# Performance work log

Hardware: AMD Instinct MI355X
Metric: run time of the kernel (lower is better)

## Reference

```python
import jax, jax.numpy as jnp
import numpy as np
import math

B, L, DIM = 2, 2048, 1024
HEADS = 16
DH = DIM // HEADS  # 64
M_IALSH = 2
U_IALSH = 0.75
NEG = -1e4  # additive mask value for non-matching hash buckets


def setup_inputs() -> dict:
    key = jax.random.key(0)
    k0, k1, k2, k3 = jax.random.split(key, 4)
    return {
        "hidden_states": jax.random.normal(k0, (B, L, DIM), jnp.float32),
        "qk_w": jax.random.normal(k1, (DIM, DIM), jnp.float32) * 0.02,
        "qk_b": jnp.zeros((DIM,), jnp.float32),
        "v_w": jax.random.normal(k2, (DIM, DIM), jnp.float32) * 0.02,
        "v_b": jnp.zeros((DIM,), jnp.float32),
        "hash_a": jax.random.normal(k3, (DH + M_IALSH,), jnp.float32),
    }


def _ialsh_mask(qkh, hash_a):
    # qkh: (b, h, l, dh). IALSH (Improved Asymmetric LSH for MIPS):
    # keys scaled so max norm per (b,h) is U; P(x)=[x, 1/2-||x||^2, 1/2-||x||^4]
    # queries unit-normalized;        Q(x)=[x/||x||, 0, 0]
    norms = jnp.linalg.norm(qkh, axis=-1, keepdims=True)          # (b,h,l,1)
    max_norm = jnp.max(norms, axis=2, keepdims=True)              # (b,h,1,1)
    xk = qkh * (U_IALSH / jnp.maximum(max_norm, 1e-12))
    nk2 = jnp.sum(xk * xk, axis=-1, keepdims=True)                # ||x||^2
    P = jnp.concatenate([xk, 0.5 - nk2, 0.5 - nk2 * nk2], axis=-1)
    q_unit = qkh / jnp.maximum(norms, 1e-12)
    zeros = jnp.zeros_like(nk2)
    Q = jnp.concatenate([q_unit, zeros, zeros], axis=-1)
    hq = (Q @ hash_a) >= 0.0                                      # (b,h,l) sign hash
    hk = (P @ hash_a) >= 0.0
    same = hq[..., :, None] == hk[..., None, :]                   # (b,h,l,l)
    return jnp.where(same, 0.0, NEG).astype(qkh.dtype)


def reference(hidden_states, qk_w, qk_b, v_w, v_b, hash_a):
    b, l, d = hidden_states.shape
    qk = hidden_states @ qk_w.T + qk_b                            # shared Q/K projection
    v = hidden_states @ v_w.T + v_b

    def split(x):  # (b,l,d) -> (b,h,l,dh)
        return x.reshape(b, l, HEADS, DH).transpose(0, 2, 1, 3)

    qkh, vh = split(qk), split(v)
    scores = jnp.einsum('bhqd,bhkd->bhqk', qkh, qkh) / math.sqrt(DH)
    scores = scores + _ialsh_mask(qkh, hash_a)
    probs = jax.nn.softmax(scores, axis=-1)  # dropout = identity (eval mode)
    ctx = jnp.einsum('bhqk,bhkd->bhqd', probs, vh)
    return ctx.transpose(0, 2, 1, 3).reshape(b, l, d)
```

## Files before the change

### kernel.cpp

```cpp
#include <hip/hip_runtime.h>

typedef unsigned short u16;
typedef unsigned char  u8;
typedef unsigned int   u32;
typedef unsigned long long u64;

typedef short bf16x8 __attribute__((ext_vector_type(8)));
typedef float f32x4  __attribute__((ext_vector_type(4)));
typedef float f32x16 __attribute__((ext_vector_type(16)));

#define DEV __device__ __forceinline__

#if __has_builtin(__builtin_amdgcn_exp2f)
#define EXP2(x) __builtin_amdgcn_exp2f(x)
#else
#define EXP2(x) exp2f(x)
#endif

DEV u16 f2bf(float x) {
  u32 u = __builtin_bit_cast(u32, x);
  u32 r = (u + 0x7fffu + ((u >> 16) & 1u)) >> 16;
  return (u16)r;
}
DEV float bf2f(u16 h) {
  u32 u = ((u32)h) << 16;
  return __builtin_bit_cast(float, u);
}
DEV f32x4 mfma16(bf16x8 a, bf16x8 b, f32x4 c) {
  return __builtin_amdgcn_mfma_f32_16x16x32_bf16(a, b, c, 0, 0, 0);
}
DEV f32x16 mfma32(bf16x8 a, bf16x8 b, f32x16 c) {
  return __builtin_amdgcn_mfma_f32_32x32x16_bf16(a, b, c, 0, 0, 0);
}
DEV u32 cvtpk(float lo, float hi) {
  u32 r;
  asm("v_cvt_pk_bf16_f32 %0, %1, %2" : "=v"(r) : "v"(lo), "v"(hi));
  return r;
}
DEV void pswap(u32& x, u32& y) {
  asm("v_permlane32_swap_b32 %0, %1" : "+v"(x), "+v"(y));
}
DEV bf16x8 mkfrag(u32 w0, u32 w1, u32 w2, u32 w3) {
  union { u32 w[4]; bf16x8 v; } u;
  u.w[0] = w0; u.w[1] = w1; u.w[2] = w2; u.w[3] = w3;
  return u.v;
}

#define GLDS(gptr, lptr)                                                  \
  __builtin_amdgcn_global_load_lds(                                       \
      (const __attribute__((address_space(1))) void*)(gptr),              \
      (__attribute__((address_space(3))) void*)(lptr), 16, 0, 0)

__global__ __launch_bounds__(256) void split3_kernel(
    const float* __restrict__ hid, const float* __restrict__ wq,
    const float* __restrict__ wv,
    u16* __restrict__ hHi, u16* __restrict__ hLo,
    u16* __restrict__ wqHi, u16* __restrict__ wqLo, u16* __restrict__ wvHi) {
  const int NH = 4194304, NW = 1048576;
  int i = blockIdx.x * 256 + threadIdx.x;
  if (i < NH) {
    float v = hid[i];
    u16 t = f2bf(v);
    hHi[i] = t;
    hLo[i] = f2bf(v - bf2f(t));
  } else if (i < NH + NW) {
    int j = i - NH;
    float v = wq[j];
    u16 t = f2bf(v);
    wqHi[j] = t;
    wqLo[j] = f2bf(v - bf2f(t));
  } else {
    int j = i - NH - NW;
    wvHi[j] = f2bf(wv[j]);
  }
}

__global__ __launch_bounds__(256) void ca_kernel(
    const float* __restrict__ W, const float* __restrict__ ha, double* __restrict__ ca) {
  int idx = blockIdx.x * 256 + threadIdx.x;
  int h = idx >> 10, k = idx & 1023;
  double s = 0.0;
#pragma unroll 8
  for (int j = 0; j < 64; ++j)
    s += (double)W[(size_t)(h * 64 + j) * 1024 + k] * (double)ha[j];
  ca[idx] = s;
}

__global__ __launch_bounds__(256) void d_kernel(
    const float* __restrict__ hid, const double* __restrict__ ca, float* __restrict__ dq) {
  const int row0 = blockIdx.x * 8 + (threadIdx.x >> 6) * 2;
  const int lane = threadIdx.x & 63;
  double a0[16], a1[16];
#pragma unroll
  for (int h = 0; h < 16; ++h) { a0[h] = 0.0; a1[h] = 0.0; }
  const float* hp = hid + (size_t)row0 * 1024;
  for (int k = lane; k < 1024; k += 64) {
    const double h0 = (double)hp[k];
    const double h1 = (double)hp[k + 1024];
#pragma unroll
    for (int h = 0; h < 16; ++h) {
      const double c = ca[h * 1024 + k];
      a0[h] += h0 * c;
      a1[h] += h1 * c;
    }
  }
#pragma unroll
  for (int h = 0; h < 16; ++h) {
    double v0 = a0[h], v1 = a1[h];
#pragma unroll
    for (int off = 32; off; off >>= 1) {
      v0 += __shfl_xor(v0, off, 64);
      v1 += __shfl_xor(v1, off, 64);
    }
    if (lane == 0) {
      const int b0 = row0 >> 11, l0 = row0 & 2047;
      dq[(size_t)(b0 * 16 + h) * 2048 + l0] = (float)v0;
      const int r1 = row0 + 1;
      dq[(size_t)((r1 >> 11) * 16 + h) * 2048 + (r1 & 2047)] = (float)v1;
    }
  }
}

__global__ __launch_bounds__(256, 2) void gemm_fused(
    const u16* __restrict__ hHi, const u16* __restrict__ hLo,
    const u16* __restrict__ wqHi, const u16* __restrict__ wqLo,
    const u16* __restrict__ wvHi,
    const float* __restrict__ qk_b, const float* __restrict__ v_b,
    u16* __restrict__ qkB, u16* __restrict__ vT, float* __restrict__ n2A) {
  constexpr int K = 1024;
  __shared__ u16 S[2][16384];
  const int tid = threadIdx.x, wave = tid >> 6, lane = tid & 63;
  const int quad = lane >> 4, lm = lane & 15;
  const int wr = wave >> 1, wc = wave & 1;
  const int m0 = blockIdx.x * 64, n0 = blockIdx.y * 128;
  const int ch = lane & 3, rA = lane >> 2;

  auto stage = [&](int kt, int buf) {
    const int k0 = kt * 32;
    const int rowA = wave * 16 + rA;
    GLDS(hHi + (size_t)(m0 + rowA) * K + k0 + ch * 8, &S[buf][0 + wave * 512]);
    GLDS(hLo + (size_t)(m0 + rowA) * K + k0 + ch * 8, &S[buf][2048 + wave * 512]);
#pragma unroll
    for (int it = 0; it < 2; ++it) {
      const int rb = wave * 2 + it;
      const int row = rb * 16 + rA;
      GLDS(wqHi + (size_t)(n0 + row) * K + k0 + ch * 8, &S[buf][4096 + rb * 512]);
      GLDS(wqLo + (size_t)(n0 + row) * K + k0 + ch * 8, &S[buf][8192 + rb * 512]);
      GLDS(wvHi + (size_t)(n0 + row) * K + k0 + ch * 8, &S[buf][12288 + rb * 512]);
    }
  };

  f32x4 aq[2][4], av[4][2];
#pragma unroll
  for (int i = 0; i < 2; ++i)
#pragma unroll
    for (int j = 0; j < 4; ++j) aq[i][j] = {0.f, 0.f, 0.f, 0.f};
#pragma unroll
  for (int i = 0; i < 4; ++i)
#pragma unroll
    for (int j = 0; j < 2; ++j) av[i][j] = {0.f, 0.f, 0.f, 0.f};

  stage(0, 0);
  __syncthreads();

  for (int kt = 0; kt < 32; ++kt) {
    const int cur = kt & 1;
    if (kt < 31) stage(kt + 1, cur ^ 1);

    bf16x8 a_h[2], a_l[2], b_h[4], b_l[4], w_h[4];
#pragma unroll
    for (int i = 0; i < 2; ++i) {
      a_h[i] = *(const bf16x8*)&S[cur][(wr * 32 + i * 16 + lm) * 32 + quad * 8];
      a_l[i] = *(const bf16x8*)&S[cur][2048 + (wr * 32 + i * 16 + lm) * 32 + quad * 8];
    }
#pragma unroll
    for (int j = 0; j < 4; ++j) {
      b_h[j] = *(const bf16x8*)&S[cur][4096 + (wc * 64 + j * 16 + lm) * 32 + quad * 8];
      b_l[j] = *(const bf16x8*)&S[cur][8192 + (wc * 64 + j * 16 + lm) * 32 + quad * 8];
      w_h[j] = *(const bf16x8*)&S[cur][12288 + (wc * 64 + j * 16 + lm) * 32 + quad * 8];
    }
#pragma unroll
    for (int i = 0; i < 2; ++i)
#pragma unroll
      for (int j = 0; j < 4; ++j) {
        aq[i][j] = mfma16(a_h[i], b_h[j], aq[i][j]);
        aq[i][j] = mfma16(a_h[i], b_l[j], aq[i][j]);
        aq[i][j] = mfma16(a_l[i], b_h[j], aq[i][j]);
      }
#pragma unroll
    for (int iv = 0; iv < 4; ++iv)
#pragma unroll
      for (int jv = 0; jv < 2; ++jv)
        av[iv][jv] = mfma16(w_h[iv], a_h[jv], av[iv][jv]);

    __syncthreads();
  }

  const int hidx = blockIdx.y * 2 + wc;
#pragma unroll
  for (int i = 0; i < 2; ++i) {
    float nn[4] = {0.f, 0.f, 0.f, 0.f};
#pragma unroll
    for (int j = 0; j < 4; ++j) {
      const int col = n0 + wc * 64 + j * 16 + lm;
      const float bv = qk_b[col];
#pragma unroll
      for (int r = 0; r < 4; ++r) {
        const int row = m0 + wr * 32 + i * 16 + quad * 4 + r;
        const float val = aq[i][j][r] + bv;
        qkB[(size_t)row * 1024 + col] = f2bf(val);
        nn[r] += val * val;
      }
    }
#pragma unroll
    for (int r = 0; r < 4; ++r)
#pragma unroll
      for (int off = 1; off < 16; off <<= 1) nn[r] += __shfl_xor(nn[r], off, 64);
    if (lm == 0) {
      const int row = m0 + wr * 32 + i * 16 + quad * 4;
      const int b = row >> 11, l = row & 2047;
      *(float4*)&n2A[(size_t)(b * 16 + hidx) * 2048 + l] =
          make_float4(nn[0], nn[1], nn[2], nn[3]);
    }
  }
#pragma unroll
  for (int iv = 0; iv < 4; ++iv)
#pragma unroll
    for (int r = 0; r < 4; ++r) {
      const int vcol = n0 + wc * 64 + iv * 16 + quad * 4 + r;
      const float bv = v_b[vcol];
#pragma unroll
      for (int jv = 0; jv < 2; ++jv) {
        const int tok = m0 + wr * 32 + jv * 16 + lm;
        vT[(size_t)vcol * 4096 + tok] = f2bf(av[iv][jv][r] + bv);
      }
    }
}

__global__ __launch_bounds__(256) void bits_kernel(
    const float* __restrict__ n2A, const float* __restrict__ dq,
    const float* __restrict__ ha, u8* __restrict__ hqA, u64* __restrict__ hkM) {
  const int bh = blockIdx.x;
  const int tid = threadIdx.x;
  const int wave = tid >> 6, lane = tid & 63;
  __shared__ float red[4];
  const float* n2p = n2A + (size_t)bh * 2048;
  float4 v0 = ((const float4*)n2p)[tid];
  float4 v1 = ((const float4*)n2p)[tid + 256];
  float lmax = fmaxf(fmaxf(fmaxf(v0.x, v0.y), fmaxf(v0.z, v0.w)),
                     fmaxf(fmaxf(v1.x, v1.y), fmaxf(v1.z, v1.w)));
#pragma unroll
  for (int off = 1; off < 64; off <<= 1) lmax = fmaxf(lmax, __shfl_xor(lmax, off, 64));
  if (lane == 0) red[wave] = lmax;
  __syncthreads();
  const float maxn2 = fmaxf(fmaxf(red[0], red[1]), fmaxf(red[2], red[3]));
  const float s = 0.75f / fmaxf(sqrtf(maxn2), 1e-12f);
  const float a64 = ha[64], a65 = ha[65];
#pragma unroll
  for (int it = 0; it < 8; ++it) {
    const int l = it * 256 + tid;
    const float dv = dq[(size_t)bh * 2048 + l];
    const float n2 = n2p[l];
    const float nk2 = s * s * n2;
    const float hkdot = s * dv + (0.5f - nk2) * a64 + (0.5f - nk2 * nk2) * a65;
    hqA[(size_t)bh * 2048 + l] = (dv >= 0.f) ? 1 : 0;
    const u64 m = __ballot(hkdot >= 0.f);
    if (lane == 0) hkM[(size_t)bh * 32 + it * 4 + wave] = m;
  }
}

__global__ __launch_bounds__(128, 2) void attn_kernel(
    const u16* __restrict__ qkb, const u16* __restrict__ vT,
    const u8* __restrict__ hqA, const u64* __restrict__ hkM,
    float* __restrict__ out) {
  __shared__ u16 Ks[2][4096];
  __shared__ u16 Vs[2][4096];

  const int id = blockIdx.x;
  const int bh = id & 31, qt = id >> 5;
  const int b = bh >> 4, h = bh & 15;
  const int tid = threadIdx.x, wave = tid >> 6, lane = tid & 63;
  const int col = lane & 31;
  const int hf = lane >> 5;
  const int ch7 = col & 7;
  const int r8 = lane >> 3, ch = lane & 7;
  const int q0 = qt * 64;
  const int token = q0 + wave * 32 + col;

  const u16* qbase = qkb + (size_t)b * 2048 * 1024 + h * 64;
  const u16* vtb = vT + (size_t)h * 64 * 4096 + b * 2048;
  const u64* hkp = hkM + (size_t)bh * 32;

  bf16x8 aQ[4];
#pragma unroll
  for (int c = 0; c < 4; ++c)
    aQ[c] = *(const bf16x8*)(qbase + (size_t)token * 1024 + c * 16 + hf * 8);
  const u32 hqx = hqA[(size_t)bh * 2048 + token] ? 0xFFFFFFFFu : 0u;

  const int srow = wave * 32;
  auto stage = [&](int kt, int buf) {
#pragma unroll
    for (int i = 0; i < 4; ++i) {
      const int row = srow + i * 8 + r8;
      const int sw = (ch ^ (row & 7)) * 8;
      GLDS(qbase + (size_t)(kt * 64 + row) * 1024 + sw, &Ks[buf][(srow + i * 8) * 64]);
      GLDS(vtb + (size_t)row * 4096 + kt * 64 + sw, &Vs[buf][(srow + i * 8) * 64]);
    }
  };

  f32x16 acc[2];
  f32x16 accLv;
#pragma unroll
  for (int r = 0; r < 16; ++r) { acc[0][r] = 0.f; acc[1][r] = 0.f; accLv[r] = 0.f; }
  const bf16x8 ones = {0x3F80, 0x3F80, 0x3F80, 0x3F80, 0x3F80, 0x3F80, 0x3F80, 0x3F80};

  const float SCL = 0.18033688f;
  const float M0 = -4.3280854f;

  u64 mk = hkp[0];
  stage(0, 0);
  __syncthreads();

  for (int kt = 0; kt < 32; ++kt) {
    const int cur = kt & 1;
    if (kt < 31) stage(kt + 1, cur ^ 1);
    const u64 mk_next = (kt < 31) ? hkp[kt + 1] : 0ull;

    const u64 msh = mk >> (hf * 4);
    u32 mw[2];
    mw[0] = (u32)msh;
    mw[1] = (u32)(msh >> 32);

#pragma unroll
    for (int kb = 0; kb < 2; ++kb) {
      const u32 hw = mw[kb] ^ hqx;
      f32x16 cs;
#pragma unroll
      for (int r = 0; r < 16; ++r) cs[r] = 0.f;
#pragma unroll
      for (int c = 0; c < 4; ++c) {
        const bf16x8 aK = *(const bf16x8*)
            &Ks[cur][(kb * 32 + col) * 64 + (((c * 2 + hf) ^ ch7) * 8)];
        cs = mfma32(aK, aQ[c], cs);
      }
      u32 pk[8];
#pragma unroll
      for (int i = 0; i < 8; ++i) {
        const int r0 = 2 * i, r1 = 2 * i + 1;
        const int pos0 = (r0 & 3) + 8 * (r0 >> 2);
        const int pos1 = (r1 & 3) + 8 * (r1 >> 2);
        float p0 = EXP2(__builtin_fmaf(cs[r0], SCL, M0));
        float p1 = EXP2(__builtin_fmaf(cs[r1], SCL, M0));
        p0 = ((hw >> pos0) & 1u) ? 0.f : p0;
        p1 = ((hw >> pos1) & 1u) ? 0.f : p1;
        pk[i] = cvtpk(p0, p1);
      }
      pswap(pk[0], pk[2]);
      pswap(pk[1], pk[3]);
      pswap(pk[4], pk[6]);
      pswap(pk[5], pk[7]);
      const bf16x8 fr0 = mkfrag(pk[0], pk[1], pk[2], pk[3]);
      const bf16x8 fr1 = mkfrag(pk[4], pk[5], pk[6], pk[7]);

      accLv = mfma32(ones, fr0, accLv);
      accLv = mfma32(ones, fr1, accLv);

#pragma unroll
      for (int db = 0; db < 2; ++db) {
        const bf16x8 aV0 = *(const bf16x8*)
            &Vs[cur][(db * 32 + col) * 64 + ((((kb * 2 + 0) * 2 + hf) ^ ch7) * 8)];
        acc[db] = mfma32(aV0, fr0, acc[db]);
        const bf16x8 aV1 = *(const bf16x8*)
            &Vs[cur][(db * 32 + col) * 64 + ((((kb * 2 + 1) * 2 + hf) ^ ch7) * 8)];
        acc[db] = mfma32(aV1, fr1, acc[db]);
      }
    }

    mk = mk_next;
    __syncthreads();
  }

  const float inv = 1.0f / accLv[0];
  float* op = out + (size_t)(b * 2048 + token) * 1024 + h * 64 + hf * 4;
#pragma unroll
  for (int db = 0; db < 2; ++db)
#pragma unroll
    for (int g = 0; g < 4; ++g) {
      float4 v4 = make_float4(acc[db][g * 4 + 0] * inv, acc[db][g * 4 + 1] * inv,
                              acc[db][g * 4 + 2] * inv, acc[db][g * 4 + 3] * inv);
      *(float4*)(op + db * 32 + g * 8) = v4;
    }
}

extern "C" void kernel_launch(void* const* d_in, const int* in_sizes, int n_in,
                              void* d_out, int out_size, void* d_ws, size_t ws_size,
                              hipStream_t stream) {
  const float* hidden = (const float*)d_in[0];
  const float* qk_w   = (const float*)d_in[1];
  const float* qk_b   = (const float*)d_in[2];
  const float* v_w    = (const float*)d_in[3];
  const float* v_b    = (const float*)d_in[4];
  const float* hash_a = (const float*)d_in[5];
  float* out = (float*)d_out;

  char* base = (char*)d_ws;
  size_t off = 0;
  auto take = [&](size_t bytes) -> char* {
    char* r = base + off;
    off += (bytes + 255) & ~(size_t)255;
    return r;
  };
  const size_t NH = 4194304;
  const size_t NW = 1048576;
  u16* hHi  = (u16*)take(NH * 2);
  u16* hLo  = (u16*)take(NH * 2);
  u16* wqHi = (u16*)take(NW * 2);
  u16* wqLo = (u16*)take(NW * 2);
  u16* wvHi = (u16*)take(NW * 2);
  u16* qkB  = (u16*)take(NH * 2);
  u16* vT   = (u16*)take(NH * 2);
  double* ca = (double*)take(16 * 1024 * 8);
  float* dq  = (float*)take(65536 * 4);
  float* n2A = (float*)take(65536 * 4);
  u8* hqA = (u8*)take(65536);
  u64* hkM = (u64*)take(32 * 32 * 8);

  hipLaunchKernelGGL(split3_kernel, dim3((NH + 2 * NW) / 256), dim3(256), 0, stream,
                     hidden, qk_w, v_w, hHi, hLo, wqHi, wqLo, wvHi);
  hipLaunchKernelGGL(ca_kernel, dim3(64), dim3(256), 0, stream, qk_w, hash_a, ca);
  hipLaunchKernelGGL(d_kernel, dim3(512), dim3(256), 0, stream, hidden, ca, dq);
  hipLaunchKernelGGL(gemm_fused, dim3(64, 8), dim3(256), 0, stream,
                     hHi, hLo, wqHi, wqLo, wvHi, qk_b, v_b, qkB, vT, n2A);
  hipLaunchKernelGGL(bits_kernel, dim3(32), dim3(256), 0, stream, n2A, dq, hash_a, hqA, hkM);
  hipLaunchKernelGGL(attn_kernel, dim3(1024), dim3(128), 0, stream, qkB, vT, hqA, hkM, out);
}
```

Before: 223.3 us.

## Process two query groups per wave in attention to reuse K/V tiles

Each attention block now covers 128 queries instead of 64. Every wave handles two 32-query groups that share the same K and V fragments loaded from LDS, and the grid is halved. The row-sum is now built from the VALU sum of probabilities plus one cross-half shuffle, replacing the extra MFMA against a ones vector. This cuts LDS traffic and global K/V staging per query, at the cost of more registers and fewer blocks, which may reduce occupancy.

```diff
diff --git a/kernel.cpp b/kernel.cpp
--- a/kernel.cpp
+++ b/kernel.cpp
@@ -284,18 +284,23 @@
   const int hf = lane >> 5;
   const int ch7 = col & 7;
   const int r8 = lane >> 3, ch = lane & 7;
-  const int q0 = qt * 64;
-  const int token = q0 + wave * 32 + col;
+  const int q0 = qt * 128;
+  const int tok0 = q0 + wave * 64 + col;
 
   const u16* qbase = qkb + (size_t)b * 2048 * 1024 + h * 64;
   const u16* vtb = vT + (size_t)h * 64 * 4096 + b * 2048;
   const u64* hkp = hkM + (size_t)bh * 32;
 
-  bf16x8 aQ[4];
-#pragma unroll
-  for (int c = 0; c < 4; ++c)
-    aQ[c] = *(const bf16x8*)(qbase + (size_t)token * 1024 + c * 16 + hf * 8);
-  const u32 hqx = hqA[(size_t)bh * 2048 + token] ? 0xFFFFFFFFu : 0u;
+  bf16x8 aQ[2][4];
+  u32 hqx[2];
+#pragma unroll
+  for (int g = 0; g < 2; ++g) {
+#pragma unroll
+    for (int c = 0; c < 4; ++c)
+      aQ[g][c] = *(const bf16x8*)(qbase +
+          (size_t)(tok0 + g * 32) * 1024 + c * 16 + hf * 8);
+    hqx[g] = hqA[(size_t)bh * 2048 + tok0 + g * 32] ? 0xFFFFFFFFu : 0u;
+  }
 
   const int srow = wave * 32;
   auto stage = [&](int kt, int buf) {
@@ -308,11 +313,14 @@
     }
   };
 
-  f32x16 acc[2];
-  f32x16 accLv;
-#pragma unroll
-  for (int r = 0; r < 16; ++r) { acc[0][r] = 0.f; acc[1][r] = 0.f; accLv[r] = 0.f; }
-  const bf16x8 ones = {0x3F80, 0x3F80, 0x3F80, 0x3F80, 0x3F80, 0x3F80, 0x3F80, 0x3F80};
+  f32x16 acc[2][2];
+#pragma unroll
+  for (int d = 0; d < 2; ++d)
+#pragma unroll
+    for (int g = 0; g < 2; ++g)
+#pragma unroll
+      for (int r = 0; r < 16; ++r) acc[d][g][r] = 0.f;
+  float accL[2] = {0.f, 0.f};
 
   const float SCL = 0.18033688f;
   const float M0 = -4.3280854f;
@@ -333,46 +341,58 @@
 
 #pragma unroll
     for (int kb = 0; kb < 2; ++kb) {
-      const u32 hw = mw[kb] ^ hqx;
-      f32x16 cs;
-#pragma unroll
-      for (int r = 0; r < 16; ++r) cs[r] = 0.f;
+      bf16x8 aK[4];
+#pragma unroll
+      for (int c = 0; c < 4; ++c)
+        aK[c] = *(const bf16x8*)
+            &Ks[cur][(kb * 32 + col) * 64 + (((c * 2 + hf) ^ ch7) * 8)];
+
+      f32x16 cs0, cs1;
+#pragma unroll
+      for (int r = 0; r < 16; ++r) { cs0[r] = 0.f; cs1[r] = 0.f; }
 #pragma unroll
       for (int c = 0; c < 4; ++c) {
-        const bf16x8 aK = *(const bf16x8*)
-            &Ks[cur][(kb * 32 + col) * 64 + (((c * 2 + hf) ^ ch7) * 8)];
-        cs = mfma32(aK, aQ[c], cs);
-      }
-      u32 pk[8];
-#pragma unroll
-      for (int i = 0; i < 8; ++i) {
-        const int r0 = 2 * i, r1 = 2 * i + 1;
-        const int pos0 = (r0 & 3) + 8 * (r0 >> 2);
-        const int pos1 = (r1 & 3) + 8 * (r1 >> 2);
-        float p0 = EXP2(__builtin_fmaf(cs[r0], SCL, M0));
-        float p1 = EXP2(__builtin_fmaf(cs[r1], SCL, M0));
-        p0 = ((hw >> pos0) & 1u) ? 0.f : p0;
-        p1 = ((hw >> pos1) & 1u) ? 0.f : p1;
-        pk[i] = cvtpk(p0, p1);
-      }
-      pswap(pk[0], pk[2]);
-      pswap(pk[1], pk[3]);
-      pswap(pk[4], pk[6]);
-      pswap(pk[5], pk[7]);
-      const bf16x8 fr0 = mkfrag(pk[0], pk[1], pk[2], pk[3]);
-      const bf16x8 fr1 = mkfrag(pk[4], pk[5], pk[6], pk[7]);
-
-      accLv = mfma32(ones, fr0, accLv);
-      accLv = mfma32(ones, fr1, accLv);
+        cs0 = mfma32(aK[c], aQ[0][c], cs0);
+        cs1 = mfma32(aK[c], aQ[1][c], cs1);
+      }
+
+      bf16x8 fr[2][2];
+#pragma unroll
+      for (int g = 0; g < 2; ++g) {
+        const u32 hw = mw[kb] ^ hqx[g];
+        u32 pk[8];
+#pragma unroll
+        for (int i = 0; i < 8; ++i) {
+          const int r0 = 2 * i, r1 = 2 * i + 1;
+          const int pos0 = (r0 & 3) + 8 * (r0 >> 2);
+          const int pos1 = (r1 & 3) + 8 * (r1 >> 2);
+          const float c0 = (g == 0) ? cs0[r0] : cs1[r0];
+          const float c1 = (g == 0) ? cs0[r1] : cs1[r1];
+          float p0 = EXP2(__builtin_fmaf(c0, SCL, M0));
+          float p1 = EXP2(__builtin_fmaf(c1, SCL, M0));
+          p0 = ((hw >> pos0) & 1u) ? 0.f : p0;
+          p1 = ((hw >> pos1) & 1u) ? 0.f : p1;
+          accL[g] += p0 + p1;
+          pk[i] = cvtpk(p0, p1);
+        }
+        pswap(pk[0], pk[2]);
+        pswap(pk[1], pk[3]);
+        pswap(pk[4], pk[6]);
+        pswap(pk[5], pk[7]);
+        fr[g][0] = mkfrag(pk[0], pk[1], pk[2], pk[3]);
+        fr[g][1] = mkfrag(pk[4], pk[5], pk[6], pk[7]);
+      }
 
 #pragma unroll
       for (int db = 0; db < 2; ++db) {
         const bf16x8 aV0 = *(const bf16x8*)
             &Vs[cur][(db * 32 + col) * 64 + ((((kb * 2 + 0) * 2 + hf) ^ ch7) * 8)];
-        acc[db] = mfma32(aV0, fr0, acc[db]);
+        acc[db][0] = mfma32(aV0, fr[0][0], acc[db][0]);
+        acc[db][1] = mfma32(aV0, fr[1][0], acc[db][1]);
         const bf16x8 aV1 = *(const bf16x8*)
             &Vs[cur][(db * 32 + col) * 64 + ((((kb * 2 + 1) * 2 + hf) ^ ch7) * 8)];
-        acc[db] = mfma32(aV1, fr1, acc[db]);
+        acc[db][0] = mfma32(aV1, fr[0][1], acc[db][0]);
+        acc[db][1] = mfma32(aV1, fr[1][1], acc[db][1]);
       }
     }
 
@@ -380,16 +400,23 @@
     __syncthreads();
   }
 
-  const float inv = 1.0f / accLv[0];
-  float* op = out + (size_t)(b * 2048 + token) * 1024 + h * 64 + hf * 4;
-#pragma unroll
-  for (int db = 0; db < 2; ++db)
-#pragma unroll
-    for (int g = 0; g < 4; ++g) {
-      float4 v4 = make_float4(acc[db][g * 4 + 0] * inv, acc[db][g * 4 + 1] * inv,
-                              acc[db][g * 4 + 2] * inv, acc[db][g * 4 + 3] * inv);
-      *(float4*)(op + db * 32 + g * 8) = v4;
-    }
+#pragma unroll
+  for (int g = 0; g < 2; ++g) {
+    float lg = accL[g];
+    lg += __shfl_xor(lg, 32);
+    const float inv = 1.0f / lg;
+    float* op = out + (size_t)(b * 2048 + tok0 + g * 32) * 1024 + h * 64 + hf * 4;
+#pragma unroll
+    for (int db = 0; db < 2; ++db)
+#pragma unroll
+      for (int gg = 0; gg < 4; ++gg) {
+        float4 v4 = make_float4(acc[db][g][gg * 4 + 0] * inv,
+                                acc[db][g][gg * 4 + 1] * inv,
+                                acc[db][g][gg * 4 + 2] * inv,
+                                acc[db][g][gg * 4 + 3] * inv);
+        *(float4*)(op + db * 32 + gg * 8) = v4;
+      }
+  }
 }
 
 extern "C" void kernel_launch(void* const* d_in, const int* in_sizes, int n_in,
@@ -432,5 +459,5 @@
   hipLaunchKernelGGL(gemm_fused, dim3(64, 8), dim3(256), 0, stream,
                      hHi, hLo, wqHi, wqLo, wvHi, qk_b, v_b, qkB, vT, n2A);
   hipLaunchKernelGGL(bits_kernel, dim3(32), dim3(256), 0, stream, n2A, dq, hash_a, hqA, hkM);
-  hipLaunchKernelGGL(attn_kernel, dim3(1024), dim3(128), 0, stream, qkB, vT, hqA, hkM, out);
-}
+  hipLaunchKernelGGL(attn_kernel, dim3(512), dim3(128), 0, stream, qkB, vT, hqA, hkM, out);
+}
```

Measured after the change: 265.7 us. 19.0% more time.
